# Performance work log

Hardware: AMD Instinct MI355X
Metric: run time of the kernel (lower is better)

The kernel has to match this reference:

```python
import jax, jax.numpy as jnp
import numpy as np

POOL_LEN = 256
EPS = 1e-5
WEIGHT_BITS = 2


def adaptive_avg_pool1d(x, out_len):
    """Faithful torch AdaptiveAvgPool1d: window i = [floor(i*L/out), ceil((i+1)*L/out)).
    Implemented via cumsum + static gathers (jit-friendly, vectorized)."""
    L = x.shape[-1]
    i = np.arange(out_len)
    starts = (i * L) // out_len
    ends = -((-(i + 1) * L) // out_len)  # integer ceil
    csum = jnp.cumsum(x, axis=-1)
    csum = jnp.concatenate([jnp.zeros(x.shape[:-1] + (1,), x.dtype), csum], axis=-1)
    counts = jnp.asarray(ends - starts, x.dtype)
    return (csum[..., ends] - csum[..., starts]) / counts


def quantize_weight(w, bits=WEIGHT_BITS):
    """2-bit symmetric uniform quantization, per-output-channel scale, STE."""
    qp = 2 ** (bits - 1) - 1          # +1
    qn = -(2 ** (bits - 1))           # -2
    scale = jnp.maximum(jnp.max(jnp.abs(w), axis=1, keepdims=True) / qp, 1e-8)
    w_q = jnp.clip(jnp.round(w / scale), qn, qp) * scale
    return w + jax.lax.stop_gradient(w_q - w)  # straight-through estimator


def setup_inputs() -> dict:
    key = jax.random.key(0)
    k1, k2, k3, kw = jax.random.split(key, 4)
    B = 64
    return {
        "stage1": jax.random.normal(k1, (B, 256, 5000), jnp.float32),
        "stage2": jax.random.normal(k2, (B, 128, 2500), jnp.float32),
        "stage3": jax.random.normal(k3, (B, 64, 625), jnp.float32),
        "alpha": jnp.ones((3,), jnp.float32) / 3.0,
        "weight": jax.random.normal(kw, (128, 448), jnp.float32) * 0.05,
        "bias": jnp.zeros((128,), jnp.float32),
        "gamma": jnp.ones((128,), jnp.float32),
        "beta": jnp.zeros((128,), jnp.float32),
    }


def reference(stage1, stage2, stage3, alpha, weight, bias, gamma, beta):
    w = jax.nn.softmax(alpha)
    s1 = adaptive_avg_pool1d(stage1, POOL_LEN) * w[0]
    s2 = adaptive_avg_pool1d(stage2, POOL_LEN) * w[1]
    s3 = adaptive_avg_pool1d(stage3, POOL_LEN) * w[2]
    fused = jnp.concatenate([s1, s2, s3], axis=1)  # (B, 448, 256)
    wq = quantize_weight(weight)
    y = jnp.einsum('oc,bcl->bol', wq, fused) + bias[None, :, None]  # (B, 128, 256)
    # BatchNorm1d (training mode: batch stats over N and L)
    mean = jnp.mean(y, axis=(0, 2))
    var = jnp.var(y, axis=(0, 2))
    yn = (y - mean[None, :, None]) * jax.lax.rsqrt(var + EPS)[None, :, None]
    yn = yn * gamma[None, :, None] + beta[None, :, None]
    act = jax.nn.elu(yn)
    return jnp.mean(act, axis=-1)  # (B, 128)
```

## Files before the change

kernel.cpp:

```cpp
#include <hip/hip_runtime.h>
#include <hip/hip_bf16.h>

#define EPSV 1e-5f

typedef __attribute__((ext_vector_type(8))) short short8v;
typedef __attribute__((ext_vector_type(4))) float float4v;

__device__ inline unsigned short f2bf(float x) {
  __hip_bfloat16 h = __float2bfloat16(x);
  return *reinterpret_cast<unsigned short*>(&h);
}

template <int BF>
__global__ __launch_bounds__(256) void pool_kernel(
    const float* __restrict__ s1, const float* __restrict__ s2,
    const float* __restrict__ s3, const float* __restrict__ alpha,
    void* __restrict__ fused_out) {
  __shared__ float row[5000];
  int rid = blockIdx.x;
  int b = rid / 448;
  int cg = rid % 448;
  const float* src; int C, L, c, widx;
  if (cg < 256)      { src = s1; C = 256; L = 5000; c = cg;       widx = 0; }
  else if (cg < 384) { src = s2; C = 128; L = 2500; c = cg - 256; widx = 1; }
  else               { src = s3; C = 64;  L = 625;  c = cg - 384; widx = 2; }

  float a0 = alpha[0], a1 = alpha[1], a2 = alpha[2];
  float mx = fmaxf(a0, fmaxf(a1, a2));
  float e0 = expf(a0 - mx), e1 = expf(a1 - mx), e2 = expf(a2 - mx);
  float wst = ((widx == 0) ? e0 : (widx == 1) ? e1 : e2) / (e0 + e1 + e2);

  const float* rowp = src + ((size_t)b * C + c) * L;
  if ((L & 3) == 0) {
    const float4* rp4 = (const float4*)rowp;
    int L4 = L >> 2;
    for (int i = threadIdx.x; i < L4; i += 256) {
      float4 v = rp4[i];
      int j = i << 2;
      row[j] = v.x; row[j + 1] = v.y; row[j + 2] = v.z; row[j + 3] = v.w;
    }
  } else {
    for (int i = threadIdx.x; i < L; i += 256) row[i] = rowp[i];
  }
  __syncthreads();

  int l = threadIdx.x;
  int start = (l * L) >> 8;
  int end = ((l + 1) * L + 255) >> 8;
  float s = 0.f;
  for (int i = start; i < end; ++i) s += row[i];
  float v = s / (float)(end - start) * wst;
  size_t oidx = ((size_t)b * 448 + cg) * 256 + l;
  if (BF) {
    ((unsigned short*)fused_out)[oidx] = f2bf(v);
  } else {
    ((float*)fused_out)[oidx] = v;
  }
}

__global__ __launch_bounds__(256) void quant_bf_kernel(
    const float* __restrict__ w, unsigned short* __restrict__ qbf,
    float* __restrict__ scales) {
  int o = blockIdx.x;
  int t = threadIdx.x;
  const float* wr = w + o * 448;
  float m = 0.f;
  for (int c = t; c < 448; c += 256) m = fmaxf(m, fabsf(wr[c]));
  __shared__ float sm[4];
  for (int off = 32; off; off >>= 1) m = fmaxf(m, __shfl_down(m, off, 64));
  if ((t & 63) == 0) sm[t >> 6] = m;
  __syncthreads();
  m = fmaxf(fmaxf(sm[0], sm[1]), fmaxf(sm[2], sm[3]));
  float scale = fmaxf(m, 1e-8f);
  for (int c = t; c < 448; c += 256) {
    float q = rintf(wr[c] / scale);
    q = fminf(fmaxf(q, -2.f), 1.f);
    qbf[o * 448 + c] = f2bf(q);
  }
  if (t == 0) scales[o] = scale;
}

__global__ __launch_bounds__(256) void quant_kernel(
    const float* __restrict__ w, float* __restrict__ wq) {
  int o = blockIdx.x;
  int t = threadIdx.x;
  const float* wr = w + o * 448;
  float m = 0.f;
  for (int c = t; c < 448; c += 256) m = fmaxf(m, fabsf(wr[c]));
  __shared__ float sm[4];
  for (int off = 32; off; off >>= 1) m = fmaxf(m, __shfl_down(m, off, 64));
  if ((t & 63) == 0) sm[t >> 6] = m;
  __syncthreads();
  m = fmaxf(fmaxf(sm[0], sm[1]), fmaxf(sm[2], sm[3]));
  float scale = fmaxf(m, 1e-8f);
  for (int c = t; c < 448; c += 256) {
    float q = rintf(wr[c] / scale);
    q = fminf(fmaxf(q, -2.f), 1.f);
    wq[o * 448 + c] = q * scale;
  }
}

__global__ __launch_bounds__(256) void mfma_gemm_kernel(
    const unsigned short* __restrict__ qbf, const float* __restrict__ scales,
    const unsigned short* __restrict__ fusedb, const float* __restrict__ bias,
    float* __restrict__ y, float* __restrict__ Psum, float* __restrict__ Pssq) {
  __shared__ __align__(16) unsigned short Asm[64][40];
  __shared__ __align__(16) unsigned short Bsm[32][66];
  int b = blockIdx.z;
  int o0 = blockIdx.y * 64;
  int l0 = blockIdx.x * 64;
  int tid = threadIdx.x;
  int wave = tid >> 6, lane = tid & 63;
  int wm = wave >> 1, wn = wave & 1;
  int lrow = lane & 15, lg = lane >> 4;
  const unsigned short* Fp = fusedb + (size_t)b * 448 * 256;

  float4v acc[2][2];
  #pragma unroll
  for (int i = 0; i < 2; ++i)
    #pragma unroll
    for (int j = 0; j < 2; ++j)
      acc[i][j] = (float4v){0.f, 0.f, 0.f, 0.f};

  for (int c0 = 0; c0 < 448; c0 += 32) {
    {
      int r = tid >> 2, k0 = (tid & 3) * 8;
      short8v v = *(const short8v*)(qbf + (size_t)(o0 + r) * 448 + c0 + k0);
      *(short8v*)&Asm[r][k0] = v;
    }
    {
      int k = tid >> 3, n0 = (tid & 7) * 8;
      short8v v = *(const short8v*)(Fp + (size_t)(c0 + k) * 256 + l0 + n0);
      *(short8v*)&Bsm[k][n0] = v;
    }
    __syncthreads();

    short8v af[2];
    #pragma unroll
    for (int mf = 0; mf < 2; ++mf)
      af[mf] = *(const short8v*)&Asm[wm * 32 + mf * 16 + lrow][lg * 8];

    #pragma unroll
    for (int nf = 0; nf < 2; ++nf) {
      int n = wn * 32 + nf * 16 + lrow;
      short8v bf;
      #pragma unroll
      for (int j = 0; j < 8; ++j) bf[j] = (short)Bsm[lg * 8 + j][n];
      #pragma unroll
      for (int mf = 0; mf < 2; ++mf)
        acc[mf][nf] = __builtin_amdgcn_mfma_f32_16x16x32_bf16(af[mf], bf, acc[mf][nf], 0, 0, 0);
    }
    __syncthreads();
  }

  float sv[2][4], qv[2][4];
  #pragma unroll
  for (int mf = 0; mf < 2; ++mf) {
    #pragma unroll
    for (int reg = 0; reg < 4; ++reg) {
      int r = o0 + wm * 32 + mf * 16 + lg * 4 + reg;
      float sc = scales[r], bv = bias[r];
      float s = 0.f, q = 0.f;
      #pragma unroll
      for (int nf = 0; nf < 2; ++nf) {
        int col = l0 + wn * 32 + nf * 16 + lrow;
        float val = acc[mf][nf][reg] * sc + bv;
        y[((size_t)b * 128 + r) * 256 + col] = val;
        s += val; q += val * val;
      }
      sv[mf][reg] = s; qv[mf][reg] = q;
    }
  }
  #pragma unroll
  for (int mf = 0; mf < 2; ++mf)
    #pragma unroll
    for (int reg = 0; reg < 4; ++reg) {
      #pragma unroll
      for (int m = 1; m < 16; m <<= 1) {
        sv[mf][reg] += __shfl_xor(sv[mf][reg], m, 64);
        qv[mf][reg] += __shfl_xor(qv[mf][reg], m, 64);
      }
    }
  if (lrow == 0) {
    int slot = b * 8 + blockIdx.x * 2 + wn;
    #pragma unroll
    for (int mf = 0; mf < 2; ++mf)
      #pragma unroll
      for (int reg = 0; reg < 4; ++reg) {
        int r = o0 + wm * 32 + mf * 16 + lg * 4 + reg;
        Psum[r * 512 + slot] = sv[mf][reg];
        Pssq[r * 512 + slot] = qv[mf][reg];
      }
  }
}

#define BM 64
#define BN 64
#define BK 16
__global__ __launch_bounds__(256) void gemm_kernel(
    const float* __restrict__ wq, const float* __restrict__ fused,
    const float* __restrict__ bias, float* __restrict__ y) {
  __shared__ float As[BK][BM + 4];
  __shared__ float Bs[BK][BN + 4];
  int b = blockIdx.z;
  int o0 = blockIdx.y * BM;
  int l0 = blockIdx.x * BN;
  const float* Bp = fused + (size_t)b * 448 * 256;
  int tid = threadIdx.x;
  int tx = tid & 15, ty = tid >> 4;
  float acc[4][4] = {};
  for (int c0 = 0; c0 < 448; c0 += BK) {
    {
      int m = tid >> 2;
      int k = (tid & 3) * 4;
      const float* p = wq + (o0 + m) * 448 + c0 + k;
      As[k][m] = p[0]; As[k + 1][m] = p[1]; As[k + 2][m] = p[2]; As[k + 3][m] = p[3];
    }
    {
      #pragma unroll
      for (int i = 0; i < 4; ++i) {
        int e = tid + 256 * i;
        int n = e & 63, k = e >> 6;
        Bs[k][n] = Bp[(size_t)(c0 + k) * 256 + l0 + n];
      }
    }
    __syncthreads();
    #pragma unroll
    for (int k = 0; k < BK; ++k) {
      float a[4], bb[4];
      #pragma unroll
      for (int i = 0; i < 4; ++i) a[i] = As[k][ty * 4 + i];
      #pragma unroll
      for (int j = 0; j < 4; ++j) bb[j] = Bs[k][tx * 4 + j];
      #pragma unroll
      for (int i = 0; i < 4; ++i)
        #pragma unroll
        for (int j = 0; j < 4; ++j)
          acc[i][j] += a[i] * bb[j];
    }
    __syncthreads();
  }
  #pragma unroll
  for (int i = 0; i < 4; ++i) {
    float bv = bias[o0 + ty * 4 + i];
    #pragma unroll
    for (int j = 0; j < 4; ++j)
      y[((size_t)b * 128 + o0 + ty * 4 + i) * 256 + l0 + tx * 4 + j] = acc[i][j] + bv;
  }
}

__global__ __launch_bounds__(256) void finalize_kernel(
    const float* __restrict__ Psum, const float* __restrict__ Pssq,
    float* __restrict__ stats) {
  int o = blockIdx.x;
  int t = threadIdx.x;
  float s = Psum[o * 512 + t] + Psum[o * 512 + 256 + t];
  float q = Pssq[o * 512 + t] + Pssq[o * 512 + 256 + t];
  __shared__ float sb[8];
  for (int m = 32; m; m >>= 1) { s += __shfl_down(s, m, 64); q += __shfl_down(q, m, 64); }
  if ((t & 63) == 0) { sb[t >> 6] = s; sb[4 + (t >> 6)] = q; }
  __syncthreads();
  if (t == 0) {
    s = sb[0] + sb[1] + sb[2] + sb[3];
    q = sb[4] + sb[5] + sb[6] + sb[7];
    float mean = s * (1.f / 16384.f);
    float var = q * (1.f / 16384.f) - mean * mean;
    stats[o] = mean;
    stats[128 + o] = rsqrtf(var + EPSV);
  }
}

__global__ __launch_bounds__(256) void stats_kernel(
    const float* __restrict__ y, float* __restrict__ stats) {
  int o = blockIdx.x;
  int l = threadIdx.x;
  float s = 0.f, ss = 0.f;
  for (int b = 0; b < 64; ++b) {
    float v = y[((size_t)b * 128 + o) * 256 + l];
    s += v; ss += v * v;
  }
  __shared__ float sbuf[8];
  for (int off = 32; off; off >>= 1) {
    s += __shfl_down(s, off, 64);
    ss += __shfl_down(ss, off, 64);
  }
  if ((l & 63) == 0) { sbuf[l >> 6] = s; sbuf[4 + (l >> 6)] = ss; }
  __syncthreads();
  if (l == 0) {
    s = sbuf[0] + sbuf[1] + sbuf[2] + sbuf[3];
    ss = sbuf[4] + sbuf[5] + sbuf[6] + sbuf[7];
    float mean = s * (1.f / 16384.f);
    float var = ss * (1.f / 16384.f) - mean * mean;
    stats[o] = mean;
    stats[128 + o] = rsqrtf(var + EPSV);
  }
}

__global__ __launch_bounds__(256) void final_kernel(
    const float* __restrict__ y, const float* __restrict__ stats,
    const float* __restrict__ gamma, const float* __restrict__ beta,
    float* __restrict__ out) {
  int w = threadIdx.x >> 6;
  int lane = threadIdx.x & 63;
  int bo = blockIdx.x * 4 + w;
  int o = bo & 127;
  float mean = stats[o], rs = stats[128 + o];
  float g = gamma[o], bt = beta[o];
  float4 v = *(const float4*)(y + (size_t)bo * 256 + lane * 4);
  float acc = 0.f;
  #pragma unroll
  for (int j = 0; j < 4; ++j) {
    float e = (&v.x)[j];
    float yn = (e - mean) * rs * g + bt;
    acc += yn > 0.f ? yn : expm1f(yn);
  }
  for (int m = 32; m; m >>= 1) acc += __shfl_down(acc, m, 64);
  if (lane == 0) out[bo] = acc * (1.f / 256.f);
}

extern "C" void kernel_launch(void* const* d_in, const int* in_sizes, int n_in,
                              void* d_out, int out_size, void* d_ws, size_t ws_size,
                              hipStream_t stream) {
  const float* s1     = (const float*)d_in[0];
  const float* s2     = (const float*)d_in[1];
  const float* s3     = (const float*)d_in[2];
  const float* alpha  = (const float*)d_in[3];
  const float* weight = (const float*)d_in[4];
  const float* bias   = (const float*)d_in[5];
  const float* gamma  = (const float*)d_in[6];
  const float* beta   = (const float*)d_in[7];
  float* out = (float*)d_out;

  char* ws = (char*)d_ws;
  unsigned short* fusedb = (unsigned short*)ws;
  unsigned short* qbf    = (unsigned short*)(ws + 14680064);
  float* scales          = (float*)(ws + 14794752);
  float* y               = (float*)(ws + 14795264);
  float* stats           = (float*)(ws + 23183872);
  float* Psum            = (float*)(ws + 23184896);
  float* Pssq            = (float*)(ws + 23447040);
  const size_t NEED_MFMA = 23709184;

  if (ws_size >= NEED_MFMA) {
    pool_kernel<1><<<64 * 448, 256, 0, stream>>>(s1, s2, s3, alpha, fusedb);
    quant_bf_kernel<<<128, 256, 0, stream>>>(weight, qbf, scales);
    dim3 g(4, 2, 64);
    mfma_gemm_kernel<<<g, 256, 0, stream>>>(qbf, scales, fusedb, bias, y, Psum, Pssq);
    finalize_kernel<<<128, 256, 0, stream>>>(Psum, Pssq, stats);
    final_kernel<<<2048, 256, 0, stream>>>(y, stats, gamma, beta, out);
  } else {
    float* fused = (float*)ws;
    float* wq    = (float*)(ws + 29360128);
    float* yf    = (float*)(ws + 29589504);
    float* st    = (float*)(ws + 37978112);
    pool_kernel<0><<<64 * 448, 256, 0, stream>>>(s1, s2, s3, alpha, fused);
    quant_kernel<<<128, 256, 0, stream>>>(weight, wq);
    dim3 g(4, 2, 64);
    gemm_kernel<<<g, 256, 0, stream>>>(wq, fused, bias, yf);
    stats_kernel<<<128, 256, 0, stream>>>(yf, st);
    final_kernel<<<2048, 256, 0, stream>>>(yf, st, gamma, beta, out);
  }
}
```

Measured before the change: 108.7 us.

## Fuse GEMM, batchnorm stats and ELU-mean into one cooperative grid-sync kernel

```diff
diff --git a/kernel.cpp b/kernel.cpp
--- a/kernel.cpp
+++ b/kernel.cpp
@@ -1,5 +1,8 @@
 #include <hip/hip_runtime.h>
 #include <hip/hip_bf16.h>
+#include <hip/hip_cooperative_groups.h>
+
+namespace cg = cooperative_groups;
 
 #define EPSV 1e-5f
 
@@ -11,19 +14,41 @@
   return *reinterpret_cast<unsigned short*>(&h);
 }
 
-template <int BF>
-__global__ __launch_bounds__(256) void pool_kernel(
+__global__ __launch_bounds__(256) void pool_quant_kernel(
     const float* __restrict__ s1, const float* __restrict__ s2,
     const float* __restrict__ s3, const float* __restrict__ alpha,
-    void* __restrict__ fused_out) {
+    const float* __restrict__ w, unsigned short* __restrict__ fusedb,
+    unsigned short* __restrict__ qbf, float* __restrict__ scales) {
   __shared__ float row[5000];
-  int rid = blockIdx.x;
-  int b = rid / 448;
-  int cg = rid % 448;
+  int bid = blockIdx.x;
+  int t = threadIdx.x;
+
+  if (bid >= 28672) {
+    int o = bid - 28672;
+    const float* wr = w + o * 448;
+    float m = 0.f;
+    for (int c = t; c < 448; c += 256) m = fmaxf(m, fabsf(wr[c]));
+    float* sm = row;
+    for (int off = 32; off; off >>= 1) m = fmaxf(m, __shfl_down(m, off, 64));
+    if ((t & 63) == 0) sm[t >> 6] = m;
+    __syncthreads();
+    m = fmaxf(fmaxf(sm[0], sm[1]), fmaxf(sm[2], sm[3]));
+    float scale = fmaxf(m, 1e-8f);
+    for (int c = t; c < 448; c += 256) {
+      float q = rintf(wr[c] / scale);
+      q = fminf(fmaxf(q, -2.f), 1.f);
+      qbf[o * 448 + c] = f2bf(q);
+    }
+    if (t == 0) scales[o] = scale;
+    return;
+  }
+
+  int b = bid / 448;
+  int cg_ = bid % 448;
   const float* src; int C, L, c, widx;
-  if (cg < 256)      { src = s1; C = 256; L = 5000; c = cg;       widx = 0; }
-  else if (cg < 384) { src = s2; C = 128; L = 2500; c = cg - 256; widx = 1; }
-  else               { src = s3; C = 64;  L = 625;  c = cg - 384; widx = 2; }
+  if (cg_ < 256)      { src = s1; C = 256; L = 5000; c = cg_;       widx = 0; }
+  else if (cg_ < 384) { src = s2; C = 128; L = 2500; c = cg_ - 256; widx = 1; }
+  else                { src = s3; C = 64;  L = 625;  c = cg_ - 384; widx = 2; }
 
   float a0 = alpha[0], a1 = alpha[1], a2 = alpha[2];
   float mx = fmaxf(a0, fmaxf(a1, a2));
@@ -34,69 +59,146 @@
   if ((L & 3) == 0) {
     const float4* rp4 = (const float4*)rowp;
     int L4 = L >> 2;
-    for (int i = threadIdx.x; i < L4; i += 256) {
+    for (int i = t; i < L4; i += 256) {
       float4 v = rp4[i];
       int j = i << 2;
       row[j] = v.x; row[j + 1] = v.y; row[j + 2] = v.z; row[j + 3] = v.w;
     }
   } else {
-    for (int i = threadIdx.x; i < L; i += 256) row[i] = rowp[i];
+    for (int i = t; i < L; i += 256) row[i] = rowp[i];
   }
   __syncthreads();
 
-  int l = threadIdx.x;
+  int l = t;
   int start = (l * L) >> 8;
   int end = ((l + 1) * L + 255) >> 8;
   float s = 0.f;
   for (int i = start; i < end; ++i) s += row[i];
   float v = s / (float)(end - start) * wst;
-  size_t oidx = ((size_t)b * 448 + cg) * 256 + l;
-  if (BF) {
-    ((unsigned short*)fused_out)[oidx] = f2bf(v);
-  } else {
-    ((float*)fused_out)[oidx] = v;
-  }
-}
-
-__global__ __launch_bounds__(256) void quant_bf_kernel(
-    const float* __restrict__ w, unsigned short* __restrict__ qbf,
-    float* __restrict__ scales) {
-  int o = blockIdx.x;
-  int t = threadIdx.x;
-  const float* wr = w + o * 448;
-  float m = 0.f;
-  for (int c = t; c < 448; c += 256) m = fmaxf(m, fabsf(wr[c]));
-  __shared__ float sm[4];
-  for (int off = 32; off; off >>= 1) m = fmaxf(m, __shfl_down(m, off, 64));
-  if ((t & 63) == 0) sm[t >> 6] = m;
-  __syncthreads();
-  m = fmaxf(fmaxf(sm[0], sm[1]), fmaxf(sm[2], sm[3]));
-  float scale = fmaxf(m, 1e-8f);
-  for (int c = t; c < 448; c += 256) {
-    float q = rintf(wr[c] / scale);
-    q = fminf(fmaxf(q, -2.f), 1.f);
-    qbf[o * 448 + c] = f2bf(q);
-  }
-  if (t == 0) scales[o] = scale;
-}
-
-__global__ __launch_bounds__(256) void quant_kernel(
-    const float* __restrict__ w, float* __restrict__ wq) {
-  int o = blockIdx.x;
-  int t = threadIdx.x;
-  const float* wr = w + o * 448;
-  float m = 0.f;
-  for (int c = t; c < 448; c += 256) m = fmaxf(m, fabsf(wr[c]));
-  __shared__ float sm[4];
-  for (int off = 32; off; off >>= 1) m = fmaxf(m, __shfl_down(m, off, 64));
-  if ((t & 63) == 0) sm[t >> 6] = m;
-  __syncthreads();
-  m = fmaxf(fmaxf(sm[0], sm[1]), fmaxf(sm[2], sm[3]));
-  float scale = fmaxf(m, 1e-8f);
-  for (int c = t; c < 448; c += 256) {
-    float q = rintf(wr[c] / scale);
-    q = fminf(fmaxf(q, -2.f), 1.f);
-    wq[o * 448 + c] = q * scale;
+  fusedb[((size_t)b * 448 + cg_) * 256 + l] = f2bf(v);
+}
+
+__global__ __launch_bounds__(256) void fused_tail_kernel(
+    const unsigned short* __restrict__ qbf, const float* __restrict__ scales,
+    const unsigned short* __restrict__ fusedb, const float* __restrict__ bias,
+    const float* __restrict__ gamma, const float* __restrict__ beta,
+    float* __restrict__ Psum, float* __restrict__ Pssq,
+    float* __restrict__ out) {
+  __shared__ __align__(16) unsigned short Asm[64][40];
+  __shared__ __align__(16) unsigned Bsm32[16][257];
+  __shared__ float red_s[64][4], red_q[64][4];
+  __shared__ float smean[64], srsig[64], sgam[64], sbet[64];
+
+  int b = blockIdx.x;
+  int o0 = blockIdx.y * 64;
+  int tid = threadIdx.x;
+  int wv = tid >> 6, lane = tid & 63;
+  int lrow = lane & 15, lg = lane >> 4;
+  const unsigned short* Fp = fusedb + (size_t)b * 448 * 256;
+
+  float4v acc[16];
+  #pragma unroll
+  for (int nf = 0; nf < 16; ++nf) acc[nf] = (float4v){0.f, 0.f, 0.f, 0.f};
+
+  for (int c0 = 0; c0 < 448; c0 += 32) {
+    {
+      int r = tid >> 2, k0a = (tid & 3) * 8;
+      *(short8v*)&Asm[r][k0a] =
+          *(const short8v*)(qbf + (size_t)(o0 + r) * 448 + c0 + k0a);
+    }
+    #pragma unroll
+    for (int cc = 0; cc < 2; ++cc) {
+      int ci = tid + 256 * cc;
+      int kp = ci >> 5;
+      int n0 = (ci & 31) * 8;
+      const unsigned short* g0 = Fp + (size_t)(c0 + 2 * kp) * 256 + n0;
+      short8v v0 = *(const short8v*)g0;
+      short8v v1 = *(const short8v*)(g0 + 256);
+      #pragma unroll
+      for (int j = 0; j < 8; ++j) {
+        Bsm32[kp][n0 + j] =
+            (((unsigned)(unsigned short)v1[j]) << 16) | (unsigned short)v0[j];
+      }
+    }
+    __syncthreads();
+
+    short8v af = *(const short8v*)&Asm[wv * 16 + lrow][lg * 8];
+    #pragma unroll
+    for (int nf = 0; nf < 16; ++nf) {
+      int n = nf * 16 + lrow;
+      int tmp[4];
+      tmp[0] = (int)Bsm32[lg * 4 + 0][n];
+      tmp[1] = (int)Bsm32[lg * 4 + 1][n];
+      tmp[2] = (int)Bsm32[lg * 4 + 2][n];
+      tmp[3] = (int)Bsm32[lg * 4 + 3][n];
+      short8v bf;
+      __builtin_memcpy(&bf, tmp, 16);
+      acc[nf] = __builtin_amdgcn_mfma_f32_16x16x32_bf16(af, bf, acc[nf], 0, 0, 0);
+    }
+    __syncthreads();
+  }
+
+  #pragma unroll
+  for (int reg = 0; reg < 4; ++reg) {
+    int r = o0 + wv * 16 + lg * 4 + reg;
+    float sc = scales[r], bv = bias[r];
+    float sv = 0.f, qv = 0.f;
+    #pragma unroll
+    for (int nf = 0; nf < 16; ++nf) {
+      float v = acc[nf][reg] * sc + bv;
+      acc[nf][reg] = v;
+      sv += v; qv += v * v;
+    }
+    #pragma unroll
+    for (int m = 1; m < 16; m <<= 1) {
+      sv += __shfl_xor(sv, m, 64);
+      qv += __shfl_xor(qv, m, 64);
+    }
+    if (lrow == 0) {
+      Psum[(size_t)r * 64 + b] = sv;
+      Pssq[(size_t)r * 64 + b] = qv;
+    }
+  }
+
+  __threadfence();
+  cg::this_grid().sync();
+
+  {
+    int ch = tid >> 2, part = tid & 3;
+    const float* Pp = Psum + (size_t)(o0 + ch) * 64 + part * 16;
+    const float* Qp = Pssq + (size_t)(o0 + ch) * 64 + part * 16;
+    float s = 0.f, q = 0.f;
+    #pragma unroll
+    for (int i = 0; i < 16; ++i) { s += Pp[i]; q += Qp[i]; }
+    red_s[ch][part] = s; red_q[ch][part] = q;
+    __syncthreads();
+    if (tid < 64) {
+      float S = red_s[tid][0] + red_s[tid][1] + red_s[tid][2] + red_s[tid][3];
+      float Q = red_q[tid][0] + red_q[tid][1] + red_q[tid][2] + red_q[tid][3];
+      float mean = S * (1.f / 16384.f);
+      float var = Q * (1.f / 16384.f) - mean * mean;
+      smean[tid] = mean;
+      srsig[tid] = rsqrtf(var + EPSV);
+      sgam[tid] = gamma[o0 + tid];
+      sbet[tid] = beta[o0 + tid];
+    }
+    __syncthreads();
+  }
+
+  #pragma unroll
+  for (int reg = 0; reg < 4; ++reg) {
+    int chl = wv * 16 + lg * 4 + reg;
+    float a = srsig[chl] * sgam[chl];
+    float bb = sbet[chl] - smean[chl] * a;
+    float es = 0.f;
+    #pragma unroll
+    for (int nf = 0; nf < 16; ++nf) {
+      float yn = acc[nf][reg] * a + bb;
+      es += yn > 0.f ? yn : expm1f(yn);
+    }
+    #pragma unroll
+    for (int m = 1; m < 16; m <<= 1) es += __shfl_xor(es, m, 64);
+    if (lrow == 0) out[(size_t)b * 128 + o0 + chl] = es * (1.f / 256.f);
   }
 }
 
@@ -114,32 +216,22 @@
   int wm = wave >> 1, wn = wave & 1;
   int lrow = lane & 15, lg = lane >> 4;
   const unsigned short* Fp = fusedb + (size_t)b * 448 * 256;
-
   float4v acc[2][2];
   #pragma unroll
   for (int i = 0; i < 2; ++i)
     #pragma unroll
-    for (int j = 0; j < 2; ++j)
-      acc[i][j] = (float4v){0.f, 0.f, 0.f, 0.f};
-
+    for (int j = 0; j < 2; ++j) acc[i][j] = (float4v){0.f, 0.f, 0.f, 0.f};
   for (int c0 = 0; c0 < 448; c0 += 32) {
-    {
-      int r = tid >> 2, k0 = (tid & 3) * 8;
-      short8v v = *(const short8v*)(qbf + (size_t)(o0 + r) * 448 + c0 + k0);
-      *(short8v*)&Asm[r][k0] = v;
-    }
-    {
-      int k = tid >> 3, n0 = (tid & 7) * 8;
+    { int r = tid >> 2, k0 = (tid & 3) * 8;
+      *(short8v*)&Asm[r][k0] = *(const short8v*)(qbf + (size_t)(o0 + r) * 448 + c0 + k0); }
+    { int k = tid >> 3, n0 = (tid & 7) * 8;
       short8v v = *(const short8v*)(Fp + (size_t)(c0 + k) * 256 + l0 + n0);
-      *(short8v*)&Bsm[k][n0] = v;
-    }
-    __syncthreads();
-
+      *(short8v*)&Bsm[k][n0] = v; }
+    __syncthreads();
     short8v af[2];
     #pragma unroll
     for (int mf = 0; mf < 2; ++mf)
       af[mf] = *(const short8v*)&Asm[wm * 32 + mf * 16 + lrow][lg * 8];
-
     #pragma unroll
     for (int nf = 0; nf < 2; ++nf) {
       int n = wn * 32 + nf * 16 + lrow;
@@ -152,7 +244,6 @@
     }
     __syncthreads();
   }
-
   float sv[2][4], qv[2][4];
   #pragma unroll
   for (int mf = 0; mf < 2; ++mf) {
@@ -174,13 +265,12 @@
   #pragma unroll
   for (int mf = 0; mf < 2; ++mf)
     #pragma unroll
-    for (int reg = 0; reg < 4; ++reg) {
+    for (int reg = 0; reg < 4; ++reg)
       #pragma unroll
       for (int m = 1; m < 16; m <<= 1) {
         sv[mf][reg] += __shfl_xor(sv[mf][reg], m, 64);
         qv[mf][reg] += __shfl_xor(qv[mf][reg], m, 64);
       }
-    }
   if (lrow == 0) {
     int slot = b * 8 + blockIdx.x * 2 + wn;
     #pragma unroll
@@ -191,61 +281,6 @@
         Psum[r * 512 + slot] = sv[mf][reg];
         Pssq[r * 512 + slot] = qv[mf][reg];
       }
-  }
-}
-
-#define BM 64
-#define BN 64
-#define BK 16
-__global__ __launch_bounds__(256) void gemm_kernel(
-    const float* __restrict__ wq, const float* __restrict__ fused,
-    const float* __restrict__ bias, float* __restrict__ y) {
-  __shared__ float As[BK][BM + 4];
-  __shared__ float Bs[BK][BN + 4];
-  int b = blockIdx.z;
-  int o0 = blockIdx.y * BM;
-  int l0 = blockIdx.x * BN;
-  const float* Bp = fused + (size_t)b * 448 * 256;
-  int tid = threadIdx.x;
-  int tx = tid & 15, ty = tid >> 4;
-  float acc[4][4] = {};
-  for (int c0 = 0; c0 < 448; c0 += BK) {
-    {
-      int m = tid >> 2;
-      int k = (tid & 3) * 4;
-      const float* p = wq + (o0 + m) * 448 + c0 + k;
-      As[k][m] = p[0]; As[k + 1][m] = p[1]; As[k + 2][m] = p[2]; As[k + 3][m] = p[3];
-    }
-    {
-      #pragma unroll
-      for (int i = 0; i < 4; ++i) {
-        int e = tid + 256 * i;
-        int n = e & 63, k = e >> 6;
-        Bs[k][n] = Bp[(size_t)(c0 + k) * 256 + l0 + n];
-      }
-    }
-    __syncthreads();
-    #pragma unroll
-    for (int k = 0; k < BK; ++k) {
-      float a[4], bb[4];
-      #pragma unroll
-      for (int i = 0; i < 4; ++i) a[i] = As[k][ty * 4 + i];
-      #pragma unroll
-      for (int j = 0; j < 4; ++j) bb[j] = Bs[k][tx * 4 + j];
-      #pragma unroll
-      for (int i = 0; i < 4; ++i)
-        #pragma unroll
-        for (int j = 0; j < 4; ++j)
-          acc[i][j] += a[i] * bb[j];
-    }
-    __syncthreads();
-  }
-  #pragma unroll
-  for (int i = 0; i < 4; ++i) {
-    float bv = bias[o0 + ty * 4 + i];
-    #pragma unroll
-    for (int j = 0; j < 4; ++j)
-      y[((size_t)b * 128 + o0 + ty * 4 + i) * 256 + l0 + tx * 4 + j] = acc[i][j] + bv;
   }
 }
 
@@ -270,32 +305,6 @@
   }
 }
 
-__global__ __launch_bounds__(256) void stats_kernel(
-    const float* __restrict__ y, float* __restrict__ stats) {
-  int o = blockIdx.x;
-  int l = threadIdx.x;
-  float s = 0.f, ss = 0.f;
-  for (int b = 0; b < 64; ++b) {
-    float v = y[((size_t)b * 128 + o) * 256 + l];
-    s += v; ss += v * v;
-  }
-  __shared__ float sbuf[8];
-  for (int off = 32; off; off >>= 1) {
-    s += __shfl_down(s, off, 64);
-    ss += __shfl_down(ss, off, 64);
-  }
-  if ((l & 63) == 0) { sbuf[l >> 6] = s; sbuf[4 + (l >> 6)] = ss; }
-  __syncthreads();
-  if (l == 0) {
-    s = sbuf[0] + sbuf[1] + sbuf[2] + sbuf[3];
-    ss = sbuf[4] + sbuf[5] + sbuf[6] + sbuf[7];
-    float mean = s * (1.f / 16384.f);
-    float var = ss * (1.f / 16384.f) - mean * mean;
-    stats[o] = mean;
-    stats[128 + o] = rsqrtf(var + EPSV);
-  }
-}
-
 __global__ __launch_bounds__(256) void final_kernel(
     const float* __restrict__ y, const float* __restrict__ stats,
     const float* __restrict__ gamma, const float* __restrict__ beta,
@@ -335,29 +344,33 @@
   unsigned short* fusedb = (unsigned short*)ws;
   unsigned short* qbf    = (unsigned short*)(ws + 14680064);
   float* scales          = (float*)(ws + 14794752);
-  float* y               = (float*)(ws + 14795264);
-  float* stats           = (float*)(ws + 23183872);
-  float* Psum            = (float*)(ws + 23184896);
-  float* Pssq            = (float*)(ws + 23447040);
-  const size_t NEED_MFMA = 23709184;
-
-  if (ws_size >= NEED_MFMA) {
-    pool_kernel<1><<<64 * 448, 256, 0, stream>>>(s1, s2, s3, alpha, fusedb);
-    quant_bf_kernel<<<128, 256, 0, stream>>>(weight, qbf, scales);
+  float* Psum            = (float*)(ws + 14795264);
+  float* Pssq            = (float*)(ws + 14828032);
+  float* y               = (float*)(ws + 14860800);
+  float* stats           = (float*)(ws + 23249408);
+  float* PsumL           = (float*)(ws + 23250432);
+  float* PssqL           = (float*)(ws + 23512576);
+
+  pool_quant_kernel<<<28800, 256, 0, stream>>>(s1, s2, s3, alpha, weight,
+                                               fusedb, qbf, scales);
+
+  int coop = 0;
+  hipDeviceGetAttribute(&coop, hipDeviceAttributeCooperativeLaunch, 0);
+
+  bool done = false;
+  if (coop) {
+    void* args[] = {(void*)&qbf, (void*)&scales, (void*)&fusedb, (void*)&bias,
+                    (void*)&gamma, (void*)&beta, (void*)&Psum, (void*)&Pssq,
+                    (void*)&out};
+    hipError_t err = hipLaunchCooperativeKernel(
+        (const void*)fused_tail_kernel, dim3(64, 2, 1), dim3(256, 1, 1),
+        args, 0, stream);
+    done = (err == hipSuccess);
+  }
+  if (!done) {
     dim3 g(4, 2, 64);
-    mfma_gemm_kernel<<<g, 256, 0, stream>>>(qbf, scales, fusedb, bias, y, Psum, Pssq);
-    finalize_kernel<<<128, 256, 0, stream>>>(Psum, Pssq, stats);
+    mfma_gemm_kernel<<<g, 256, 0, stream>>>(qbf, scales, fusedb, bias, y, PsumL, PssqL);
+    finalize_kernel<<<128, 256, 0, stream>>>(PsumL, PssqL, stats);
     final_kernel<<<2048, 256, 0, stream>>>(y, stats, gamma, beta, out);
-  } else {
-    float* fused = (float*)ws;
-    float* wq    = (float*)(ws + 29360128);
-    float* yf    = (float*)(ws + 29589504);
-    float* st    = (float*)(ws + 37978112);
-    pool_kernel<0><<<64 * 448, 256, 0, stream>>>(s1, s2, s3, alpha, fused);
-    quant_kernel<<<128, 256, 0, stream>>>(weight, wq);
-    dim3 g(4, 2, 64);
-    gemm_kernel<<<g, 256, 0, stream>>>(wq, fused, bias, yf);
-    stats_kernel<<<128, 256, 0, stream>>>(yf, st);
-    final_kernel<<<2048, 256, 0, stream>>>(yf, st, gamma, beta, out);
-  }
-}
+  }
+}
```

New measurement: 148.8 us. 36.9% more time.
